# Performance work log

Hardware: AMD Instinct MI355X
Metric: run time of the kernel (lower is better)

The kernel has to match this reference:

```python
import jax, jax.numpy as jnp
import numpy as np

QK_DIM = 1024
V_DIM = 1024
NUM_HEADS = 16
HEAD_DIM = 64
INNER = NUM_HEADS * HEAD_DIM  # 1024
SCALE = HEAD_DIM ** -0.5


def setup_inputs() -> dict:
    key = jax.random.key(0)
    ks = jax.random.split(key, 8)
    m, nq, nkv = 4, 2048, 2048
    xq = jax.random.normal(ks[0], (m, nq, QK_DIM), dtype=jnp.float32)
    xk = jax.random.normal(ks[1], (m, nkv, QK_DIM), dtype=jnp.float32)
    xv = jax.random.normal(ks[2], (m, nkv, V_DIM), dtype=jnp.float32)
    # torch nn.Linear weights are [out, in]; y = x @ W.T
    s_qk = (QK_DIM) ** -0.5
    s_in = (INNER) ** -0.5
    Wq = jax.random.uniform(ks[3], (INNER, QK_DIM), jnp.float32, -s_qk, s_qk)
    Wk = jax.random.uniform(ks[4], (INNER, QK_DIM), jnp.float32, -s_qk, s_qk)
    Wv = jax.random.uniform(ks[5], (INNER, V_DIM), jnp.float32, -s_qk, s_qk)
    Wo = jax.random.uniform(ks[6], (V_DIM, INNER), jnp.float32, -s_in, s_in)
    bo = jax.random.uniform(ks[7], (V_DIM,), jnp.float32, -s_in, s_in)
    return {"xq": xq, "xk": xk, "xv": xv, "Wq": Wq, "Wk": Wk, "Wv": Wv, "Wo": Wo, "bo": bo}


def reference(xq, xk, xv, Wq, Wk, Wv, Wo, bo):
    m, nq, _ = xq.shape
    nkv = xk.shape[1]
    # projections (no bias), split heads: b n (h d) -> b h n d
    q = (xq @ Wq.T).reshape(m, nq, NUM_HEADS, HEAD_DIM).transpose(0, 2, 1, 3)
    k = (xk @ Wk.T).reshape(m, nkv, NUM_HEADS, HEAD_DIM).transpose(0, 2, 1, 3)
    v = (xv @ Wv.T).reshape(m, nkv, NUM_HEADS, HEAD_DIM).transpose(0, 2, 1, 3)
    dots = jnp.einsum("bhqd,bhkd->bhqk", q, k) * SCALE  # [m,h,nq,nkv]
    attn = jax.nn.softmax(dots, axis=-1)
    out = jnp.einsum("bhqk,bhkd->bhqd", attn, v)
    out = out.transpose(0, 2, 1, 3).reshape(m, nq, INNER)  # b h n d -> b n (h d)
    return out @ Wo.T + bo  # to_out Linear (dropout p=0 -> identity)
```

## Files before the change

### kernel.cpp

```cpp
#include <hip/hip_runtime.h>

typedef unsigned short u16;
using bf16x8 = __attribute__((ext_vector_type(8))) __bf16;
using f32x4  = __attribute__((ext_vector_type(4))) float;

#define QSCALE 0.18033688011f

#define EXP2F(x) __builtin_amdgcn_exp2f(x)

__device__ __forceinline__ u16 f2bf(float f) {
  union { float f; unsigned int u; } x; x.f = f;
  unsigned int r = x.u + 0x7FFFu + ((x.u >> 16) & 1u);
  return (u16)(r >> 16);
}

__device__ __forceinline__ bf16x8 ld8(const u16* p) {
  return *reinterpret_cast<const bf16x8*>(p);
}

__device__ __forceinline__ void gload16(const u16* g, u16* l) {
  __builtin_amdgcn_global_load_lds(
      (const __attribute__((address_space(1))) unsigned int*)g,
      (__attribute__((address_space(3))) unsigned int*)l, 16, 0, 0);
}

__global__ void cast3_f32_to_bf16(const float* __restrict__ a, const float* __restrict__ b,
                                  const float* __restrict__ c, u16* __restrict__ out, int n4) {
  const int y = blockIdx.y;
  const int i = blockIdx.x * 256 + threadIdx.x;
  if (i >= n4) return;
  const float* src = (y == 0) ? a : (y == 1) ? b : c;
  const float4 v = reinterpret_cast<const float4*>(src)[i];
  ushort4 o;
  o.x = f2bf(v.x); o.y = f2bf(v.y); o.z = f2bf(v.z); o.w = f2bf(v.w);
  reinterpret_cast<ushort4*>(out + (size_t)y * n4 * 4)[i] = o;
}

__global__ void cast4_f32_to_bf16(const float* __restrict__ a, const float* __restrict__ b,
                                  const float* __restrict__ c, const float* __restrict__ d,
                                  u16* __restrict__ out, int n4) {
  const int y = blockIdx.y;
  const int i = blockIdx.x * 256 + threadIdx.x;
  if (i >= n4) return;
  const float* src = (y == 0) ? a : (y == 1) ? b : (y == 2) ? c : d;
  const float4 v = reinterpret_cast<const float4*>(src)[i];
  ushort4 o;
  o.x = f2bf(v.x); o.y = f2bf(v.y); o.z = f2bf(v.z); o.w = f2bf(v.w);
  reinterpret_cast<ushort4*>(out + (size_t)y * n4 * 4)[i] = o;
}

#define GEMM_CORE(A_, B_, K_, BX_, BY_)                                              \
  __shared__ alignas(16) u16 lds_a[128 * 32];                                        \
  __shared__ alignas(16) u16 lds_b[128 * 32];                                        \
  const int t = threadIdx.x;                                                         \
  const int w = t >> 6, lane = t & 63;                                               \
  const int wr = w >> 1, wc = w & 1;                                                 \
  const size_t row0 = (size_t)(BY_) * 128;                                           \
  const size_t col0 = (size_t)(BX_) * 128;                                           \
  f32x4 acc[4][4];                                                                   \
  _Pragma("unroll") for (int i = 0; i < 4; ++i)                                      \
    _Pragma("unroll") for (int j = 0; j < 4; ++j) acc[i][j] = {0.f, 0.f, 0.f, 0.f};  \
  const u16* ga = A_ + (row0 + (t >> 2)) * K_ + (t & 3) * 8;                         \
  const u16* gb = B_ + (col0 + (t >> 2)) * K_ + (t & 3) * 8;                         \
  u16* la = lds_a + w * 512;                                                         \
  u16* lb = lds_b + w * 512;                                                         \
  const int fr = lane & 15;                                                          \
  const int fk = (lane >> 4) * 8;                                                    \
  for (int kt = 0; kt < K_; kt += 32) {                                              \
    __syncthreads();                                                                 \
    gload16(ga + kt, la);                                                            \
    gload16(ga + (size_t)64 * K_ + kt, la + 2048);                                   \
    gload16(gb + kt, lb);                                                            \
    gload16(gb + (size_t)64 * K_ + kt, lb + 2048);                                   \
    __syncthreads();                                                                 \
    bf16x8 af[4], bfr[4];                                                            \
    _Pragma("unroll") for (int i = 0; i < 4; ++i)                                    \
      af[i] = ld8(&lds_a[(wr * 64 + i * 16 + fr) * 32 + fk]);                        \
    _Pragma("unroll") for (int j = 0; j < 4; ++j)                                    \
      bfr[j] = ld8(&lds_b[(wc * 64 + j * 16 + fr) * 32 + fk]);                       \
    _Pragma("unroll") for (int i = 0; i < 4; ++i)                                    \
      _Pragma("unroll") for (int j = 0; j < 4; ++j)                                  \
        acc[i][j] = __builtin_amdgcn_mfma_f32_16x16x32_bf16(af[i], bfr[j], acc[i][j], 0, 0, 0); \
  }                                                                                  \
  const int er = (lane >> 4) * 4, ec = lane & 15;

__global__ __launch_bounds__(256)
void gemm_qkv(const u16* __restrict__ Aall, const u16* __restrict__ Ball,
              u16* __restrict__ Call) {
  const int g = (blockIdx.x & 7) * 192 + (blockIdx.x >> 3);
  const int bx = g & 7, by = (g >> 3) & 63, z = g >> 9;
  const u16* A = Aall + (size_t)z * 8192 * 1024;
  const u16* B = Ball + (size_t)z * 1024 * 1024;
  u16* C = Call + (size_t)z * 8192 * 1024;
  GEMM_CORE(A, B, 1024, bx, by)
#pragma unroll
  for (int i = 0; i < 4; ++i)
#pragma unroll
    for (int j = 0; j < 4; ++j) {
      const size_t row = row0 + wr * 64 + i * 16 + er;
      const size_t col = col0 + wc * 64 + j * 16 + ec;
      if (z == 0) {
#pragma unroll
        for (int r = 0; r < 4; ++r)
          C[(row + r) * 1024 + col] = f2bf(acc[i][j][r] * QSCALE);
      } else if (z == 1) {
#pragma unroll
        for (int r = 0; r < 4; ++r) {
          const size_t n = row + r;
          const size_t colswz = (col & ~(size_t)63) |
                                ((col & 63) ^ (((n & 7) << 3)));
          C[n * 1024 + colswz] = f2bf(acc[i][j][r]);
        }
      } else {
        ushort4 o4;
        o4.x = f2bf(acc[i][j][0]); o4.y = f2bf(acc[i][j][1]);
        o4.z = f2bf(acc[i][j][2]); o4.w = f2bf(acc[i][j][3]);
        const size_t nloc = row & 2047;
        const size_t d = col & 63;
        size_t pos = (nloc & ~(size_t)31) | (((nloc >> 2) & 3) << 3) |
                     (((nloc >> 4) & 1) << 2) | (nloc & 3);
        pos ^= (d & 7) << 3;
        const size_t idx = (((row >> 11) * 16 + (col >> 6)) * 64 + d) * 2048 + pos;
        *reinterpret_cast<ushort4*>(&C[idx]) = o4;
      }
    }
}

__global__ __launch_bounds__(256)
void gemm_out(const u16* __restrict__ A, const u16* __restrict__ B,
              float* __restrict__ Cf, const float* __restrict__ bias) {
  const int g = (blockIdx.x & 7) * 64 + (blockIdx.x >> 3);
  const int bx = g & 7, by = g >> 3;
  GEMM_CORE(A, B, 1024, bx, by)
#pragma unroll
  for (int i = 0; i < 4; ++i)
#pragma unroll
    for (int j = 0; j < 4; ++j) {
      const size_t row = row0 + wr * 64 + i * 16 + er;
      const size_t col = col0 + wc * 64 + j * 16 + ec;
#pragma unroll
      for (int r = 0; r < 4; ++r)
        Cf[(row + r) * 1024 + col] = acc[i][j][r] + bias[col];
    }
}

__global__ __launch_bounds__(512)
void flash_attn(const u16* __restrict__ Q, const u16* __restrict__ Km,
                const u16* __restrict__ Vt, u16* __restrict__ O) {
  const int o_blk = (blockIdx.x & 7) * 64 + (blockIdx.x >> 3);
  const int qt = o_blk & 7, h = (o_blk >> 3) & 15, b = o_blk >> 7;
  const int t = threadIdx.x;
  const int w = t >> 6, lane = t & 63;
  const int l16 = lane & 15, lh = lane >> 4;

  __shared__ alignas(16) u16 kt_lds[2][64][64];
  __shared__ alignas(16) u16 vt_lds[2][64][64];

  const size_t base_qk = ((size_t)b * 2048) * 1024 + (size_t)h * 64;
  const size_t base_vt = ((size_t)(b * 16 + h)) * 64 * 2048;

  bf16x8 qf[2][2];
#pragma unroll
  for (int g = 0; g < 2; ++g) {
    const size_t qrow = (size_t)qt * 256 + (w * 2 + g) * 16 + l16;
    const u16* qp = Q + base_qk + qrow * 1024 + lh * 8;
    qf[g][0] = ld8(qp);
    qf[g][1] = ld8(qp + 32);
  }

  bf16x8 vones;
#pragma unroll
  for (int i = 0; i < 8; ++i) vones[i] = (__bf16)1.0f;

  f32x4 o_acc[2][4];
  f32x4 o_sum[2];
#pragma unroll
  for (int g = 0; g < 2; ++g) {
#pragma unroll
    for (int j = 0; j < 4; ++j) o_acc[g][j] = {0.f, 0.f, 0.f, 0.f};
    o_sum[g] = {0.f, 0.f, 0.f, 0.f};
  }

  const int srow = t >> 3;
  const int schk = (t & 7) * 8;
  const u16* kg = Km + base_qk + (size_t)srow * 1024 + schk;
  const u16* vg = Vt + base_vt + (size_t)srow * 2048 + schk;
  u16* kl0 = &kt_lds[0][0][0] + w * 512;
  u16* kl1 = &kt_lds[1][0][0] + w * 512;
  u16* vl0 = &vt_lds[0][0][0] + w * 512;
  u16* vl1 = &vt_lds[1][0][0] + w * 512;

  gload16(kg, kl0);
  gload16(vg, vl0);

  const int xo = (l16 & 7) << 3;

  for (int it = 0; it < 32; ++it) {
    const int cur = it & 1;
    __syncthreads();

    if (it != 31) {
      const int nkv = (it + 1) * 64;
      gload16(kg + (size_t)nkv * 1024, cur ? kl0 : kl1);
      gload16(vg + nkv, cur ? vl0 : vl1);
    }

    f32x4 s[2][4];
#pragma unroll
    for (int g = 0; g < 2; ++g)
#pragma unroll
      for (int j = 0; j < 4; ++j) s[g][j] = {0.f, 0.f, 0.f, 0.f};
    __builtin_amdgcn_s_setprio(1);
#pragma unroll
    for (int j = 0; j < 4; ++j)
#pragma unroll
      for (int ks = 0; ks < 2; ++ks) {
        bf16x8 kf = ld8(&kt_lds[cur][j * 16 + l16][(ks * 32 + lh * 8) ^ xo]);
        s[0][j] = __builtin_amdgcn_mfma_f32_16x16x32_bf16(kf, qf[0][ks], s[0][j], 0, 0, 0);
        s[1][j] = __builtin_amdgcn_mfma_f32_16x16x32_bf16(kf, qf[1][ks], s[1][j], 0, 0, 0);
      }
    __builtin_amdgcn_s_setprio(0);

    bf16x8 pa[2][2];
#pragma unroll
    for (int g = 0; g < 2; ++g)
#pragma unroll
      for (int j = 0; j < 4; ++j)
#pragma unroll
        for (int r = 0; r < 4; ++r)
          s[g][j][r] = EXP2F(s[g][j][r]);
#pragma unroll
    for (int g = 0; g < 2; ++g)
#pragma unroll
      for (int c = 0; c < 2; ++c)
#pragma unroll
        for (int i = 0; i < 8; ++i)
          pa[g][c][i] = (__bf16)s[g][2 * c + (i >> 2)][i & 3];

    __builtin_amdgcn_s_setprio(1);
#pragma unroll
    for (int c = 0; c < 2; ++c) {
      o_sum[0] = __builtin_amdgcn_mfma_f32_16x16x32_bf16(pa[0][c], vones, o_sum[0], 0, 0, 0);
      o_sum[1] = __builtin_amdgcn_mfma_f32_16x16x32_bf16(pa[1][c], vones, o_sum[1], 0, 0, 0);
#pragma unroll
      for (int jd = 0; jd < 4; ++jd) {
        bf16x8 vf = ld8(&vt_lds[cur][jd * 16 + l16][(c * 32 + lh * 8) ^ xo]);
        o_acc[0][jd] = __builtin_amdgcn_mfma_f32_16x16x32_bf16(pa[0][c], vf, o_acc[0][jd], 0, 0, 0);
        o_acc[1][jd] = __builtin_amdgcn_mfma_f32_16x16x32_bf16(pa[1][c], vf, o_acc[1][jd], 0, 0, 0);
      }
    }
    __builtin_amdgcn_s_setprio(0);
  }

#pragma unroll
  for (int g = 0; g < 2; ++g) {
    float linv[4];
#pragma unroll
    for (int r = 0; r < 4; ++r) linv[r] = 1.0f / o_sum[g][r];
    const size_t orow0 = (size_t)b * 2048 + (size_t)qt * 256 + (w * 2 + g) * 16;
#pragma unroll
    for (int jd = 0; jd < 4; ++jd) {
      const int col = h * 64 + jd * 16 + l16;
#pragma unroll
      for (int r = 0; r < 4; ++r)
        O[(orow0 + lh * 4 + r) * 1024 + col] = f2bf(o_acc[g][jd][r] * linv[r]);
    }
  }
}

extern "C" void kernel_launch(void* const* d_in, const int* in_sizes, int n_in,
                              void* d_out, int out_size, void* d_ws, size_t ws_size,
                              hipStream_t stream) {
  const float* xq = (const float*)d_in[0];
  const float* xk = (const float*)d_in[1];
  const float* xv = (const float*)d_in[2];
  const float* Wq = (const float*)d_in[3];
  const float* Wk = (const float*)d_in[4];
  const float* Wv = (const float*)d_in[5];
  const float* Wo = (const float*)d_in[6];
  const float* bo = (const float*)d_in[7];
  float* out = (float*)d_out;

  const size_t X = (size_t)8192 * 1024;
  const size_t W = (size_t)1024 * 1024;

  u16* p = (u16*)d_ws;
  u16* x_bf  = p; p += 3 * X;
  u16* w_bf  = p; p += 4 * W;
  u16* qkv   = p; p += 3 * X;
  u16* attn_bf = x_bf;

  dim3 blk(256);
  cast3_f32_to_bf16<<<dim3(8192, 3), blk, 0, stream>>>(xq, xk, xv, x_bf, (int)(X / 4));
  cast4_f32_to_bf16<<<dim3(1024, 4), blk, 0, stream>>>(Wq, Wk, Wv, Wo, w_bf, (int)(W / 4));

  gemm_qkv<<<dim3(1536), blk, 0, stream>>>(x_bf, w_bf, qkv);

  flash_attn<<<dim3(512), dim3(512), 0, stream>>>(qkv, qkv + X, qkv + 2 * X, attn_bf);

  gemm_out<<<dim3(512), blk, 0, stream>>>(attn_bf, w_bf + 3 * W, out, bo);
}
```

Measured before the change: 193.9 us.

## Fuse fp32-to-bf16 activation cast into QKV GEMM A-tile loads

Drops the separate cast kernel for xq/xk/xv. The QKV GEMM now reads fp32 activations directly into registers, converts them to bf16 and writes them to LDS, prefetching the next K tile in registers. This avoids a full write and re-read of a 48 MB bf16 activation copy. In exchange, each GEMM tile now reads fp32 A data at twice the bytes, possibly several times since 8 column blocks share the same rows, and adds full vmcnt waits and sched barriers. The flash attention loop also gets an explicit vmcnt(0) wait and scheduling fences around its barrier.

```diff
diff --git a/kernel.cpp b/kernel.cpp
--- a/kernel.cpp
+++ b/kernel.cpp
@@ -7,6 +7,7 @@
 #define QSCALE 0.18033688011f
 
 #define EXP2F(x) __builtin_amdgcn_exp2f(x)
+#define SCHED_FENCE() __builtin_amdgcn_sched_barrier(0)
 
 __device__ __forceinline__ u16 f2bf(float f) {
   union { float f; unsigned int u; } x; x.f = f;
@@ -22,18 +23,6 @@
   __builtin_amdgcn_global_load_lds(
       (const __attribute__((address_space(1))) unsigned int*)g,
       (__attribute__((address_space(3))) unsigned int*)l, 16, 0, 0);
-}
-
-__global__ void cast3_f32_to_bf16(const float* __restrict__ a, const float* __restrict__ b,
-                                  const float* __restrict__ c, u16* __restrict__ out, int n4) {
-  const int y = blockIdx.y;
-  const int i = blockIdx.x * 256 + threadIdx.x;
-  if (i >= n4) return;
-  const float* src = (y == 0) ? a : (y == 1) ? b : c;
-  const float4 v = reinterpret_cast<const float4*>(src)[i];
-  ushort4 o;
-  o.x = f2bf(v.x); o.y = f2bf(v.y); o.z = f2bf(v.z); o.w = f2bf(v.w);
-  reinterpret_cast<ushort4*>(out + (size_t)y * n4 * 4)[i] = o;
 }
 
 __global__ void cast4_f32_to_bf16(const float* __restrict__ a, const float* __restrict__ b,
@@ -85,14 +74,80 @@
   const int er = (lane >> 4) * 4, ec = lane & 15;
 
 __global__ __launch_bounds__(256)
-void gemm_qkv(const u16* __restrict__ Aall, const u16* __restrict__ Ball,
+void gemm_qkv(const float* __restrict__ xq, const float* __restrict__ xk,
+              const float* __restrict__ xv, const u16* __restrict__ Ball,
               u16* __restrict__ Call) {
   const int g = (blockIdx.x & 7) * 192 + (blockIdx.x >> 3);
   const int bx = g & 7, by = (g >> 3) & 63, z = g >> 9;
-  const u16* A = Aall + (size_t)z * 8192 * 1024;
+  const float* A = (z == 0) ? xq : (z == 1) ? xk : xv;
   const u16* B = Ball + (size_t)z * 1024 * 1024;
   u16* C = Call + (size_t)z * 8192 * 1024;
-  GEMM_CORE(A, B, 1024, bx, by)
+
+  __shared__ alignas(16) u16 lds_a[128 * 32];
+  __shared__ alignas(16) u16 lds_b[128 * 32];
+  const int t = threadIdx.x;
+  const int w = t >> 6, lane = t & 63;
+  const int wr = w >> 1, wc = w & 1;
+  const size_t row0 = (size_t)by * 128;
+  const size_t col0 = (size_t)bx * 128;
+
+  f32x4 acc[4][4];
+#pragma unroll
+  for (int i = 0; i < 4; ++i)
+#pragma unroll
+    for (int j = 0; j < 4; ++j) acc[i][j] = {0.f, 0.f, 0.f, 0.f};
+
+  const float* ga = A + (row0 + (t >> 2)) * 1024 + (t & 3) * 8;
+  const u16* gb = B + (col0 + (t >> 2)) * 1024 + (t & 3) * 8;
+  u16* la_w = lds_a + t * 8;
+  u16* lb = lds_b + w * 512;
+
+  const int fr = lane & 15;
+  const int fk = (lane >> 4) * 8;
+
+  float4 a0 = *reinterpret_cast<const float4*>(ga);
+  float4 a1 = *reinterpret_cast<const float4*>(ga + 4);
+  float4 a2 = *reinterpret_cast<const float4*>(ga + (size_t)64 * 1024);
+  float4 a3 = *reinterpret_cast<const float4*>(ga + (size_t)64 * 1024 + 4);
+
+  for (int kt = 0; kt < 1024; kt += 32) {
+    __syncthreads();
+    SCHED_FENCE();
+    {
+      bf16x8 aw0, aw1;
+      aw0[0] = (__bf16)a0.x; aw0[1] = (__bf16)a0.y; aw0[2] = (__bf16)a0.z; aw0[3] = (__bf16)a0.w;
+      aw0[4] = (__bf16)a1.x; aw0[5] = (__bf16)a1.y; aw0[6] = (__bf16)a1.z; aw0[7] = (__bf16)a1.w;
+      aw1[0] = (__bf16)a2.x; aw1[1] = (__bf16)a2.y; aw1[2] = (__bf16)a2.z; aw1[3] = (__bf16)a2.w;
+      aw1[4] = (__bf16)a3.x; aw1[5] = (__bf16)a3.y; aw1[6] = (__bf16)a3.z; aw1[7] = (__bf16)a3.w;
+      *reinterpret_cast<bf16x8*>(la_w) = aw0;
+      *reinterpret_cast<bf16x8*>(la_w + 2048) = aw1;
+    }
+    gload16(gb + kt, lb);
+    gload16(gb + (size_t)64 * 1024 + kt, lb + 2048);
+    asm volatile("s_waitcnt vmcnt(0) lgkmcnt(0)" ::: "memory");
+    SCHED_FENCE();
+    __syncthreads();
+    SCHED_FENCE();
+
+    const int nkt = (kt + 32) & 1023;
+    a0 = *reinterpret_cast<const float4*>(ga + nkt);
+    a1 = *reinterpret_cast<const float4*>(ga + nkt + 4);
+    a2 = *reinterpret_cast<const float4*>(ga + (size_t)64 * 1024 + nkt);
+    a3 = *reinterpret_cast<const float4*>(ga + (size_t)64 * 1024 + nkt + 4);
+
+    bf16x8 af[4], bfr[4];
+#pragma unroll
+    for (int i = 0; i < 4; ++i) af[i] = ld8(&lds_a[(wr * 64 + i * 16 + fr) * 32 + fk]);
+#pragma unroll
+    for (int j = 0; j < 4; ++j) bfr[j] = ld8(&lds_b[(wc * 64 + j * 16 + fr) * 32 + fk]);
+#pragma unroll
+    for (int i = 0; i < 4; ++i)
+#pragma unroll
+      for (int j = 0; j < 4; ++j)
+        acc[i][j] = __builtin_amdgcn_mfma_f32_16x16x32_bf16(af[i], bfr[j], acc[i][j], 0, 0, 0);
+  }
+
+  const int er = (lane >> 4) * 4, ec = lane & 15;
 #pragma unroll
   for (int i = 0; i < 4; ++i)
 #pragma unroll
@@ -197,13 +252,17 @@
 
   for (int it = 0; it < 32; ++it) {
     const int cur = it & 1;
+    asm volatile("s_waitcnt vmcnt(0)" ::: "memory");
+    SCHED_FENCE();
     __syncthreads();
+    SCHED_FENCE();
 
     if (it != 31) {
       const int nkv = (it + 1) * 64;
       gload16(kg + (size_t)nkv * 1024, cur ? kl0 : kl1);
       gload16(vg + nkv, cur ? vl0 : vl1);
     }
+    SCHED_FENCE();
 
     f32x4 s[2][4];
 #pragma unroll
@@ -285,16 +344,14 @@
   const size_t W = (size_t)1024 * 1024;
 
   u16* p = (u16*)d_ws;
-  u16* x_bf  = p; p += 3 * X;
+  u16* attn_bf = p; p += X;
   u16* w_bf  = p; p += 4 * W;
   u16* qkv   = p; p += 3 * X;
-  u16* attn_bf = x_bf;
 
   dim3 blk(256);
-  cast3_f32_to_bf16<<<dim3(8192, 3), blk, 0, stream>>>(xq, xk, xv, x_bf, (int)(X / 4));
   cast4_f32_to_bf16<<<dim3(1024, 4), blk, 0, stream>>>(Wq, Wk, Wv, Wo, w_bf, (int)(W / 4));
 
-  gemm_qkv<<<dim3(1536), blk, 0, stream>>>(x_bf, w_bf, qkv);
+  gemm_qkv<<<dim3(1536), blk, 0, stream>>>(xq, xk, xv, w_bf, qkv);
 
   flash_attn<<<dim3(512), dim3(512), 0, stream>>>(qkv, qkv + X, qkv + 2 * X, attn_bf);
 
```

Result: slower. 334.6 us (+72.6%).

## Use 256x256 double-buffered pipelined GEMM tiles and fence flash-attention loads

Applied to the files above, without the earlier changes.

Replaces the 128x128, 256-thread GEMM with a 256x256-tile, 512-thread kernel for both the QKV and output projections. The new kernel uses double-buffered, XOR-swizzled LDS with K=64 steps and issues the next tile's global-to-LDS loads between MFMA sub-steps, so each block reuses more data and overlaps loads with compute. The flash-attention loop gains an explicit vmcnt wait and scheduling barriers around its barrier and prefetch. The larger tiles cut the grid to 384 and 128 blocks, which risks poor wave balance and leaves CUs idle in the output GEMM.

```diff
diff --git a/kernel.cpp b/kernel.cpp
--- a/kernel.cpp
+++ b/kernel.cpp
@@ -7,6 +7,7 @@
 #define QSCALE 0.18033688011f
 
 #define EXP2F(x) __builtin_amdgcn_exp2f(x)
+#define SCHED_FENCE() __builtin_amdgcn_sched_barrier(0)
 
 __device__ __forceinline__ u16 f2bf(float f) {
   union { float f; unsigned int u; } x; x.f = f;
@@ -18,7 +19,7 @@
   return *reinterpret_cast<const bf16x8*>(p);
 }
 
-__device__ __forceinline__ void gload16(const u16* g, u16* l) {
+__device__ __forceinline__ void gload16(const void* g, void* l) {
   __builtin_amdgcn_global_load_lds(
       (const __attribute__((address_space(1))) unsigned int*)g,
       (__attribute__((address_space(3))) unsigned int*)l, 16, 0, 0);
@@ -49,72 +50,118 @@
   reinterpret_cast<ushort4*>(out + (size_t)y * n4 * 4)[i] = o;
 }
 
-#define GEMM_CORE(A_, B_, K_, BX_, BY_)                                              \
-  __shared__ alignas(16) u16 lds_a[128 * 32];                                        \
-  __shared__ alignas(16) u16 lds_b[128 * 32];                                        \
-  const int t = threadIdx.x;                                                         \
-  const int w = t >> 6, lane = t & 63;                                               \
-  const int wr = w >> 1, wc = w & 1;                                                 \
-  const size_t row0 = (size_t)(BY_) * 128;                                           \
-  const size_t col0 = (size_t)(BX_) * 128;                                           \
-  f32x4 acc[4][4];                                                                   \
-  _Pragma("unroll") for (int i = 0; i < 4; ++i)                                      \
-    _Pragma("unroll") for (int j = 0; j < 4; ++j) acc[i][j] = {0.f, 0.f, 0.f, 0.f};  \
-  const u16* ga = A_ + (row0 + (t >> 2)) * K_ + (t & 3) * 8;                         \
-  const u16* gb = B_ + (col0 + (t >> 2)) * K_ + (t & 3) * 8;                         \
-  u16* la = lds_a + w * 512;                                                         \
-  u16* lb = lds_b + w * 512;                                                         \
-  const int fr = lane & 15;                                                          \
-  const int fk = (lane >> 4) * 8;                                                    \
-  for (int kt = 0; kt < K_; kt += 32) {                                              \
-    __syncthreads();                                                                 \
-    gload16(ga + kt, la);                                                            \
-    gload16(ga + (size_t)64 * K_ + kt, la + 2048);                                   \
-    gload16(gb + kt, lb);                                                            \
-    gload16(gb + (size_t)64 * K_ + kt, lb + 2048);                                   \
-    __syncthreads();                                                                 \
-    bf16x8 af[4], bfr[4];                                                            \
-    _Pragma("unroll") for (int i = 0; i < 4; ++i)                                    \
-      af[i] = ld8(&lds_a[(wr * 64 + i * 16 + fr) * 32 + fk]);                        \
-    _Pragma("unroll") for (int j = 0; j < 4; ++j)                                    \
-      bfr[j] = ld8(&lds_b[(wc * 64 + j * 16 + fr) * 32 + fk]);                       \
-    _Pragma("unroll") for (int i = 0; i < 4; ++i)                                    \
-      _Pragma("unroll") for (int j = 0; j < 4; ++j)                                  \
-        acc[i][j] = __builtin_amdgcn_mfma_f32_16x16x32_bf16(af[i], bfr[j], acc[i][j], 0, 0, 0); \
-  }                                                                                  \
-  const int er = (lane >> 4) * 4, ec = lane & 15;
-
-__global__ __launch_bounds__(256)
-void gemm_qkv(const u16* __restrict__ Aall, const u16* __restrict__ Ball,
-              u16* __restrict__ Call) {
-  const int g = (blockIdx.x & 7) * 192 + (blockIdx.x >> 3);
-  const int bx = g & 7, by = (g >> 3) & 63, z = g >> 9;
+__device__ __forceinline__ void gemm8_core(const u16* __restrict__ A, const u16* __restrict__ B,
+                                           int by, int bx, f32x4 (&acc)[8][4],
+                                           u16 (*lds_a)[16384], u16 (*lds_b)[16384]) {
+  const int t = threadIdx.x;
+  const int w = t >> 6, lane = t & 63;
+  const int wm = w >> 2, wn = w & 3;
+  const int fr = lane & 15, lh = lane >> 4;
+  const int xr = (fr & 4) << 2;
+  const int kch = ((t & 7) ^ ((t >> 4) & 2)) * 8;
+
+  const u16* ga = A + (size_t)(by * 256 + (t >> 3)) * 1024 + kch;
+  const u16* gb = B + (size_t)(bx * 256 + (t >> 3)) * 1024 + kch;
+
+#pragma unroll
+  for (int m = 0; m < 8; ++m)
+#pragma unroll
+    for (int n = 0; n < 4; ++n) acc[m][n] = {0.f, 0.f, 0.f, 0.f};
+
+#pragma unroll
+  for (int q = 0; q < 4; ++q) {
+    gload16(ga + (size_t)q * 64 * 1024, &lds_a[0][q * 4096 + w * 512]);
+    gload16(gb + (size_t)q * 64 * 1024, &lds_b[0][q * 4096 + w * 512]);
+  }
+
+  for (int it = 0; it < 8; ++it) {
+    const int ts = 2 * it + 1;
+    const int tn = (2 * it + 2) & 15;
+    bf16x8 bfr[4][2];
+#pragma unroll
+    for (int p = 0; p < 8; ++p) {
+      const int b = p >> 2, q = p & 3;
+      if (q == 0) { asm volatile("s_waitcnt vmcnt(0)" ::: "memory"); }
+      __builtin_amdgcn_s_barrier();
+      if (q == 0) {
+#pragma unroll
+        for (int nn = 0; nn < 4; ++nn)
+#pragma unroll
+          for (int ks = 0; ks < 2; ++ks)
+            bfr[nn][ks] = ld8(&lds_b[b][(wn * 64 + nn * 16 + fr) * 64 + ((ks * 32 + lh * 8) ^ xr)]);
+      }
+      bf16x8 af[2][2];
+#pragma unroll
+      for (int mm = 0; mm < 2; ++mm)
+#pragma unroll
+        for (int ks = 0; ks < 2; ++ks)
+          af[mm][ks] = ld8(&lds_a[b][(wm * 128 + q * 32 + mm * 16 + fr) * 64 + ((ks * 32 + lh * 8) ^ xr)]);
+      {
+        const int tt = (p < 4) ? ts : tn;
+        const int db = (p < 4) ? 1 : 0;
+        const int q0 = (q & 1) * 2;
+        if (q < 2) {
+          gload16(gb + (size_t)(q0 + 0) * 64 * 1024 + tt * 64, &lds_b[db][(q0 + 0) * 4096 + w * 512]);
+          gload16(gb + (size_t)(q0 + 1) * 64 * 1024 + tt * 64, &lds_b[db][(q0 + 1) * 4096 + w * 512]);
+        } else {
+          gload16(ga + (size_t)(q0 + 0) * 64 * 1024 + tt * 64, &lds_a[db][(q0 + 0) * 4096 + w * 512]);
+          gload16(ga + (size_t)(q0 + 1) * 64 * 1024 + tt * 64, &lds_a[db][(q0 + 1) * 4096 + w * 512]);
+        }
+      }
+      __builtin_amdgcn_s_setprio(1);
+#pragma unroll
+      for (int nn = 0; nn < 4; ++nn)
+#pragma unroll
+        for (int mm = 0; mm < 2; ++mm)
+#pragma unroll
+          for (int ks = 0; ks < 2; ++ks)
+            acc[q * 2 + mm][nn] = __builtin_amdgcn_mfma_f32_16x16x32_bf16(
+                af[mm][ks], bfr[nn][ks], acc[q * 2 + mm][nn], 0, 0, 0);
+      __builtin_amdgcn_s_setprio(0);
+    }
+  }
+}
+
+__global__ __launch_bounds__(512)
+void gemm8_qkv(const u16* __restrict__ Aall, const u16* __restrict__ Ball,
+               u16* __restrict__ Call) {
+  __shared__ alignas(16) u16 lds_a[2][16384];
+  __shared__ alignas(16) u16 lds_b[2][16384];
+  const int g = (blockIdx.x & 7) * 48 + (blockIdx.x >> 3);
+  const int z = g >> 7, r7 = g & 127;
+  const int by = r7 >> 2, bx = r7 & 3;
   const u16* A = Aall + (size_t)z * 8192 * 1024;
   const u16* B = Ball + (size_t)z * 1024 * 1024;
   u16* C = Call + (size_t)z * 8192 * 1024;
-  GEMM_CORE(A, B, 1024, bx, by)
-#pragma unroll
-  for (int i = 0; i < 4; ++i)
-#pragma unroll
-    for (int j = 0; j < 4; ++j) {
-      const size_t row = row0 + wr * 64 + i * 16 + er;
-      const size_t col = col0 + wc * 64 + j * 16 + ec;
+
+  f32x4 acc[8][4];
+  gemm8_core(A, B, by, bx, acc, lds_a, lds_b);
+
+  const int t = threadIdx.x;
+  const int w = t >> 6, lane = t & 63;
+  const int wm = w >> 2, wn = w & 3;
+  const int er = (lane >> 4) * 4, ec = lane & 15;
+#pragma unroll
+  for (int m = 0; m < 8; ++m)
+#pragma unroll
+    for (int nn = 0; nn < 4; ++nn) {
+      const size_t row = (size_t)by * 256 + wm * 128 + m * 16 + er;
+      const size_t col = (size_t)bx * 256 + wn * 64 + nn * 16 + ec;
       if (z == 0) {
 #pragma unroll
-        for (int r = 0; r < 4; ++r)
-          C[(row + r) * 1024 + col] = f2bf(acc[i][j][r] * QSCALE);
+        for (int rr = 0; rr < 4; ++rr)
+          C[(row + rr) * 1024 + col] = f2bf(acc[m][nn][rr] * QSCALE);
       } else if (z == 1) {
 #pragma unroll
-        for (int r = 0; r < 4; ++r) {
-          const size_t n = row + r;
-          const size_t colswz = (col & ~(size_t)63) |
-                                ((col & 63) ^ (((n & 7) << 3)));
-          C[n * 1024 + colswz] = f2bf(acc[i][j][r]);
+        for (int rr = 0; rr < 4; ++rr) {
+          const size_t n = row + rr;
+          const size_t colswz = (col & ~(size_t)63) | ((col & 63) ^ ((n & 7) << 3));
+          C[n * 1024 + colswz] = f2bf(acc[m][nn][rr]);
         }
       } else {
         ushort4 o4;
-        o4.x = f2bf(acc[i][j][0]); o4.y = f2bf(acc[i][j][1]);
-        o4.z = f2bf(acc[i][j][2]); o4.w = f2bf(acc[i][j][3]);
+        o4.x = f2bf(acc[m][nn][0]); o4.y = f2bf(acc[m][nn][1]);
+        o4.z = f2bf(acc[m][nn][2]); o4.w = f2bf(acc[m][nn][3]);
         const size_t nloc = row & 2047;
         const size_t d = col & 63;
         size_t pos = (nloc & ~(size_t)31) | (((nloc >> 2) & 3) << 3) |
@@ -126,21 +173,30 @@
     }
 }
 
-__global__ __launch_bounds__(256)
-void gemm_out(const u16* __restrict__ A, const u16* __restrict__ B,
-              float* __restrict__ Cf, const float* __restrict__ bias) {
-  const int g = (blockIdx.x & 7) * 64 + (blockIdx.x >> 3);
-  const int bx = g & 7, by = g >> 3;
-  GEMM_CORE(A, B, 1024, bx, by)
-#pragma unroll
-  for (int i = 0; i < 4; ++i)
-#pragma unroll
-    for (int j = 0; j < 4; ++j) {
-      const size_t row = row0 + wr * 64 + i * 16 + er;
-      const size_t col = col0 + wc * 64 + j * 16 + ec;
-#pragma unroll
-      for (int r = 0; r < 4; ++r)
-        Cf[(row + r) * 1024 + col] = acc[i][j][r] + bias[col];
+__global__ __launch_bounds__(512)
+void gemm8_out(const u16* __restrict__ A, const u16* __restrict__ B,
+               float* __restrict__ Cf, const float* __restrict__ bias) {
+  __shared__ alignas(16) u16 lds_a[2][16384];
+  __shared__ alignas(16) u16 lds_b[2][16384];
+  const int g = (blockIdx.x & 7) * 16 + (blockIdx.x >> 3);
+  const int by = g >> 2, bx = g & 3;
+
+  f32x4 acc[8][4];
+  gemm8_core(A, B, by, bx, acc, lds_a, lds_b);
+
+  const int t = threadIdx.x;
+  const int w = t >> 6, lane = t & 63;
+  const int wm = w >> 2, wn = w & 3;
+  const int er = (lane >> 4) * 4, ec = lane & 15;
+#pragma unroll
+  for (int m = 0; m < 8; ++m)
+#pragma unroll
+    for (int nn = 0; nn < 4; ++nn) {
+      const size_t row = (size_t)by * 256 + wm * 128 + m * 16 + er;
+      const size_t col = (size_t)bx * 256 + wn * 64 + nn * 16 + ec;
+#pragma unroll
+      for (int rr = 0; rr < 4; ++rr)
+        Cf[(row + rr) * 1024 + col] = acc[m][nn][rr] + bias[col];
     }
 }
 
@@ -197,13 +253,17 @@
 
   for (int it = 0; it < 32; ++it) {
     const int cur = it & 1;
+    asm volatile("s_waitcnt vmcnt(0)" ::: "memory");
+    SCHED_FENCE();
     __syncthreads();
+    SCHED_FENCE();
 
     if (it != 31) {
       const int nkv = (it + 1) * 64;
       gload16(kg + (size_t)nkv * 1024, cur ? kl0 : kl1);
       gload16(vg + nkv, cur ? vl0 : vl1);
     }
+    SCHED_FENCE();
 
     f32x4 s[2][4];
 #pragma unroll
@@ -294,9 +354,9 @@
   cast3_f32_to_bf16<<<dim3(8192, 3), blk, 0, stream>>>(xq, xk, xv, x_bf, (int)(X / 4));
   cast4_f32_to_bf16<<<dim3(1024, 4), blk, 0, stream>>>(Wq, Wk, Wv, Wo, w_bf, (int)(W / 4));
 
-  gemm_qkv<<<dim3(1536), blk, 0, stream>>>(x_bf, w_bf, qkv);
+  gemm8_qkv<<<dim3(384), dim3(512), 0, stream>>>(x_bf, w_bf, qkv);
 
   flash_attn<<<dim3(512), dim3(512), 0, stream>>>(qkv, qkv + X, qkv + 2 * X, attn_bf);
 
-  gemm_out<<<dim3(512), blk, 0, stream>>>(attn_bf, w_bf + 3 * W, out, bo);
-}
+  gemm8_out<<<dim3(128), dim3(512), 0, stream>>>(attn_bf, w_bf + 3 * W, out, bo);
+}
```

After: 197.0 us. No clear change (+1.6%).

## Replace QKV GEMM with 8-wave 128x256 double-buffered pipelined kernel

Applied to the files above, without the earlier changes.

Rewrites the QKV projection GEMM as a 512-thread kernel with 128x256 tiles, K-step 64, double-buffered LDS, XOR-swizzled LDS layout and global-to-LDS loads interleaved between MFMA sub-steps. The aim is to hide global load latency behind MFMA work and raise reuse per tile compared with the old single-buffer 128x128 kernel. It also adds explicit vmcnt waits and scheduling barriers to the shared GEMM core and to the flash-attention loop, so loads are complete before the barriers. The larger LDS footprint (96KB) lowers occupancy, and the hand-written barrier pattern must be correct to avoid races.

```diff
diff --git a/kernel.cpp b/kernel.cpp
--- a/kernel.cpp
+++ b/kernel.cpp
@@ -7,6 +7,7 @@
 #define QSCALE 0.18033688011f
 
 #define EXP2F(x) __builtin_amdgcn_exp2f(x)
+#define SCHED_FENCE() __builtin_amdgcn_sched_barrier(0)
 
 __device__ __forceinline__ u16 f2bf(float f) {
   union { float f; unsigned int u; } x; x.f = f;
@@ -18,7 +19,7 @@
   return *reinterpret_cast<const bf16x8*>(p);
 }
 
-__device__ __forceinline__ void gload16(const u16* g, u16* l) {
+__device__ __forceinline__ void gload16(const void* g, void* l) {
   __builtin_amdgcn_global_load_lds(
       (const __attribute__((address_space(1))) unsigned int*)g,
       (__attribute__((address_space(3))) unsigned int*)l, 16, 0, 0);
@@ -72,6 +73,7 @@
     gload16(ga + (size_t)64 * K_ + kt, la + 2048);                                   \
     gload16(gb + kt, lb);                                                            \
     gload16(gb + (size_t)64 * K_ + kt, lb + 2048);                                   \
+    asm volatile("s_waitcnt vmcnt(0)" ::: "memory");                                 \
     __syncthreads();                                                                 \
     bf16x8 af[4], bfr[4];                                                            \
     _Pragma("unroll") for (int i = 0; i < 4; ++i)                                    \
@@ -84,37 +86,117 @@
   }                                                                                  \
   const int er = (lane >> 4) * 4, ec = lane & 15;
 
-__global__ __launch_bounds__(256)
-void gemm_qkv(const u16* __restrict__ Aall, const u16* __restrict__ Ball,
-              u16* __restrict__ Call) {
-  const int g = (blockIdx.x & 7) * 192 + (blockIdx.x >> 3);
-  const int bx = g & 7, by = (g >> 3) & 63, z = g >> 9;
+__device__ __forceinline__ void gemm8b_core(const u16* __restrict__ A, const u16* __restrict__ B,
+                                            int by, int bx, f32x4 (&acc)[4][4],
+                                            u16 (*lds_a)[8192], u16 (*lds_b)[16384]) {
+  const int t = threadIdx.x;
+  const int w = t >> 6, lane = t & 63;
+  const int wm = w >> 2, wn = w & 3;
+  const int fr = lane & 15, lh = lane >> 4;
+  const int xr = (fr & 4) << 2;
+  const int kch = ((t & 7) ^ ((t >> 4) & 2)) * 8;
+
+  const u16* ga = A + (size_t)(by * 128 + (t >> 3)) * 1024 + kch;
+  const u16* gb = B + (size_t)(bx * 256 + (t >> 3)) * 1024 + kch;
+
+#pragma unroll
+  for (int m = 0; m < 4; ++m)
+#pragma unroll
+    for (int n = 0; n < 4; ++n) acc[m][n] = {0.f, 0.f, 0.f, 0.f};
+
+#pragma unroll
+  for (int q = 0; q < 2; ++q)
+    gload16(ga + (size_t)q * 64 * 1024, &lds_a[0][q * 4096 + w * 512]);
+#pragma unroll
+  for (int q = 0; q < 4; ++q)
+    gload16(gb + (size_t)q * 64 * 1024, &lds_b[0][q * 4096 + w * 512]);
+
+  for (int it = 0; it < 8; ++it) {
+    const int ts = 2 * it + 1;
+    const int tn = (2 * it + 2) & 15;
+    bf16x8 bfr[4][2];
+#pragma unroll
+    for (int p = 0; p < 8; ++p) {
+      const int b = p >> 2, q = p & 3;
+      if (q == 0) { asm volatile("s_waitcnt vmcnt(0)" ::: "memory"); }
+      __builtin_amdgcn_s_barrier();
+      if (q == 0) {
+#pragma unroll
+        for (int nn = 0; nn < 4; ++nn)
+#pragma unroll
+          for (int ks = 0; ks < 2; ++ks)
+            bfr[nn][ks] = ld8(&lds_b[b][(wn * 64 + nn * 16 + fr) * 64 + ((ks * 32 + lh * 8) ^ xr)]);
+      }
+      bf16x8 af[2];
+#pragma unroll
+      for (int ks = 0; ks < 2; ++ks)
+        af[ks] = ld8(&lds_a[b][(wm * 64 + q * 16 + fr) * 64 + ((ks * 32 + lh * 8) ^ xr)]);
+      {
+        const int tt = (p < 4) ? ts : tn;
+        const int db = (p < 4) ? 1 : 0;
+        if (q == 0) {
+          gload16(gb + (size_t)0 * 64 * 1024 + tt * 64, &lds_b[db][0 * 4096 + w * 512]);
+          gload16(gb + (size_t)1 * 64 * 1024 + tt * 64, &lds_b[db][1 * 4096 + w * 512]);
+        } else if (q == 1) {
+          gload16(gb + (size_t)2 * 64 * 1024 + tt * 64, &lds_b[db][2 * 4096 + w * 512]);
+          gload16(gb + (size_t)3 * 64 * 1024 + tt * 64, &lds_b[db][3 * 4096 + w * 512]);
+        } else if (q == 2) {
+          gload16(ga + (size_t)0 * 64 * 1024 + tt * 64, &lds_a[db][0 * 4096 + w * 512]);
+        } else {
+          gload16(ga + (size_t)1 * 64 * 1024 + tt * 64, &lds_a[db][1 * 4096 + w * 512]);
+        }
+      }
+      __builtin_amdgcn_s_setprio(1);
+#pragma unroll
+      for (int nn = 0; nn < 4; ++nn)
+#pragma unroll
+        for (int ks = 0; ks < 2; ++ks)
+          acc[q][nn] = __builtin_amdgcn_mfma_f32_16x16x32_bf16(af[ks], bfr[nn][ks], acc[q][nn], 0, 0, 0);
+      __builtin_amdgcn_s_setprio(0);
+    }
+  }
+}
+
+__global__ __launch_bounds__(512)
+void gemm8_qkv(const u16* __restrict__ Aall, const u16* __restrict__ Ball,
+               u16* __restrict__ Call) {
+  __shared__ alignas(16) u16 lds_a[2][8192];
+  __shared__ alignas(16) u16 lds_b[2][16384];
+  const int g = (blockIdx.x & 7) * 96 + (blockIdx.x >> 3);
+  const int z = g >> 8, r8 = g & 255;
+  const int by = r8 >> 2, bx = r8 & 3;
   const u16* A = Aall + (size_t)z * 8192 * 1024;
   const u16* B = Ball + (size_t)z * 1024 * 1024;
   u16* C = Call + (size_t)z * 8192 * 1024;
-  GEMM_CORE(A, B, 1024, bx, by)
-#pragma unroll
-  for (int i = 0; i < 4; ++i)
-#pragma unroll
-    for (int j = 0; j < 4; ++j) {
-      const size_t row = row0 + wr * 64 + i * 16 + er;
-      const size_t col = col0 + wc * 64 + j * 16 + ec;
+
+  f32x4 acc[4][4];
+  gemm8b_core(A, B, by, bx, acc, lds_a, lds_b);
+
+  const int t = threadIdx.x;
+  const int w = t >> 6, lane = t & 63;
+  const int wm = w >> 2, wn = w & 3;
+  const int er = (lane >> 4) * 4, ec = lane & 15;
+#pragma unroll
+  for (int m = 0; m < 4; ++m)
+#pragma unroll
+    for (int nn = 0; nn < 4; ++nn) {
+      const size_t row = (size_t)by * 128 + wm * 64 + m * 16 + er;
+      const size_t col = (size_t)bx * 256 + wn * 64 + nn * 16 + ec;
       if (z == 0) {
 #pragma unroll
-        for (int r = 0; r < 4; ++r)
-          C[(row + r) * 1024 + col] = f2bf(acc[i][j][r] * QSCALE);
+        for (int rr = 0; rr < 4; ++rr)
+          C[(row + rr) * 1024 + col] = f2bf(acc[m][nn][rr] * QSCALE);
       } else if (z == 1) {
 #pragma unroll
-        for (int r = 0; r < 4; ++r) {
-          const size_t n = row + r;
-          const size_t colswz = (col & ~(size_t)63) |
-                                ((col & 63) ^ (((n & 7) << 3)));
-          C[n * 1024 + colswz] = f2bf(acc[i][j][r]);
+        for (int rr = 0; rr < 4; ++rr) {
+          const size_t n = row + rr;
+          const size_t colswz = (col & ~(size_t)63) | ((col & 63) ^ ((n & 7) << 3));
+          C[n * 1024 + colswz] = f2bf(acc[m][nn][rr]);
         }
       } else {
         ushort4 o4;
-        o4.x = f2bf(acc[i][j][0]); o4.y = f2bf(acc[i][j][1]);
-        o4.z = f2bf(acc[i][j][2]); o4.w = f2bf(acc[i][j][3]);
+        o4.x = f2bf(acc[m][nn][0]); o4.y = f2bf(acc[m][nn][1]);
+        o4.z = f2bf(acc[m][nn][2]); o4.w = f2bf(acc[m][nn][3]);
         const size_t nloc = row & 2047;
         const size_t d = col & 63;
         size_t pos = (nloc & ~(size_t)31) | (((nloc >> 2) & 3) << 3) |
@@ -197,13 +279,17 @@
 
   for (int it = 0; it < 32; ++it) {
     const int cur = it & 1;
+    asm volatile("s_waitcnt vmcnt(0)" ::: "memory");
+    SCHED_FENCE();
     __syncthreads();
+    SCHED_FENCE();
 
     if (it != 31) {
       const int nkv = (it + 1) * 64;
       gload16(kg + (size_t)nkv * 1024, cur ? kl0 : kl1);
       gload16(vg + nkv, cur ? vl0 : vl1);
     }
+    SCHED_FENCE();
 
     f32x4 s[2][4];
 #pragma unroll
@@ -294,7 +380,7 @@
   cast3_f32_to_bf16<<<dim3(8192, 3), blk, 0, stream>>>(xq, xk, xv, x_bf, (int)(X / 4));
   cast4_f32_to_bf16<<<dim3(1024, 4), blk, 0, stream>>>(Wq, Wk, Wv, Wo, w_bf, (int)(W / 4));
 
-  gemm_qkv<<<dim3(1536), blk, 0, stream>>>(x_bf, w_bf, qkv);
+  gemm8_qkv<<<dim3(768), dim3(512), 0, stream>>>(x_bf, w_bf, qkv);
 
   flash_attn<<<dim3(512), dim3(512), 0, stream>>>(qkv, qkv + X, qkv + 2 * X, attn_bf);
 
```

New measurement: 197.7 us. Within noise of the previous version (+2.0%).
